# Optimization experiments

Measured on AMD Instinct MI355X. Metric: run time of the kernel, lower is better.

Reference implementation:

```python
import jax, jax.numpy as jnp
import numpy as np

NEG = -1e6  # mask value used by d2l-style masked_softmax


def masked_softmax(scores, valid_lens):
    # scores: [B, Q, K]; valid_lens: [B] int — mask key positions j >= valid_len
    K = scores.shape[-1]
    mask = jnp.arange(K, dtype=jnp.int32)[None, None, :] < valid_lens[:, None, None]
    scores = jnp.where(mask, scores, NEG)
    return jax.nn.softmax(scores, axis=-1)


def setup_inputs() -> dict:
    key = jax.random.key(0)
    kq, kk, kv, kl = jax.random.split(key, 4)
    B, Q, K, d = 16, 4096, 4096, 128
    queries = jax.random.normal(kq, (B, Q, d), dtype=jnp.float32)
    keys = jax.random.normal(kk, (B, K, d), dtype=jnp.float32)
    values = jax.random.normal(kv, (B, K, d), dtype=jnp.float32)
    valid_lens = jax.random.randint(kl, (B,), 1, K + 1, dtype=jnp.int32)
    return {"queries": queries, "keys": keys, "values": values,
            "valid_lens": valid_lens}


def reference(queries, keys, values, valid_lens):
    d = queries.shape[-1]
    # [B, Q, K] scores = Q K^T / sqrt(d)
    scores = jnp.einsum('bqd,bkd->bqk', queries, keys) / jnp.sqrt(
        jnp.asarray(d, queries.dtype))
    attn = masked_softmax(scores, valid_lens)
    # dropout is identity in eval mode
    return jnp.einsum('bqk,bkd->bqd', attn, values)
```

## Files before the change

kernel.cpp:

```cpp
#include <hip/hip_runtime.h>
#include <stdint.h>

typedef __attribute__((ext_vector_type(8))) short short8;
typedef __attribute__((ext_vector_type(4))) float float4v;

#define B_  16
#define S_  4096
#define D_  128
#define TM  64
#define TN  64
#define NT_ (S_ / TN)
#define IMG 8192

__device__ __forceinline__ unsigned short f2bf(float f) {
    union { float f; uint32_t u; } c; c.f = f;
    uint32_t u = c.u + 0x7FFFu + ((c.u >> 16) & 1u);
    return (unsigned short)(u >> 16);
}

__device__ __forceinline__ uint4 pack8(float4v x, float4v y) {
    uint4 r;
    r.x = (uint32_t)f2bf(x[0]) | ((uint32_t)f2bf(x[1]) << 16);
    r.y = (uint32_t)f2bf(x[2]) | ((uint32_t)f2bf(x[3]) << 16);
    r.z = (uint32_t)f2bf(y[0]) | ((uint32_t)f2bf(y[1]) << 16);
    r.w = (uint32_t)f2bf(y[2]) | ((uint32_t)f2bf(y[3]) << 16);
    return r;
}

__device__ __forceinline__ void gload16(const unsigned short* g, unsigned short* l) {
    __builtin_amdgcn_global_load_lds(
        (const __attribute__((address_space(1))) unsigned int*)g,
        (__attribute__((address_space(3))) unsigned int*)l, 16, 0, 0);
}

__global__ __launch_bounds__(256)
void prepass(const float* __restrict__ Kg, const float* __restrict__ Vg,
             unsigned short* __restrict__ Kb, unsigned short* __restrict__ Vb)
{
    __shared__ __align__(16) unsigned short Vimg[IMG];
    const int t = threadIdx.x;
    const int tile = blockIdx.x, b = blockIdx.y;
    const size_t img = (size_t)(b * NT_ + tile) * IMG;

    {
        const float* src = Kg + ((size_t)b * S_ + tile * TN) * D_;
        unsigned short* dst = Kb + img;
        #pragma unroll
        for (int i = 0; i < 4; ++i) {
            int bid = i * 256 + t;
            int row = bid >> 4, cbp = bid & 15;
            int cb  = cbp ^ (row & 7);
            const float* s = src + row * D_ + cb * 8;
            float4v x = *(const float4v*)s;
            float4v y = *(const float4v*)(s + 4);
            *(uint4*)(dst + (size_t)bid * 8) = pack8(x, y);
        }
    }
    {
        const float* src = Vg + ((size_t)b * S_ + tile * TN) * D_;
        #pragma unroll
        for (int i = 0; i < 8; ++i) {
            int e = (i * 256 + t) * 4;
            int k = e >> 7, c = e & 127;
            float4v v = *(const float4v*)(src + e);
            #pragma unroll
            for (int j = 0; j < 4; ++j) {
                int dr = c + j;
                int cbp = (k >> 3) ^ (dr & 7);
                Vimg[dr * TN + cbp * 8 + (k & 7)] = f2bf(v[j]);
            }
        }
        __syncthreads();
        unsigned short* dst = Vb + img;
        #pragma unroll
        for (int i = 0; i < 4; ++i) {
            int o = (i * 256 + t) * 8;
            *(uint4*)(dst + o) = *(const uint4*)(&Vimg[o]);
        }
    }
}

__global__ __launch_bounds__(256, 4)
void attn_fwd(const float* __restrict__ Qg,
              const unsigned short* __restrict__ Kb,
              const unsigned short* __restrict__ Vb,
              const int* __restrict__ VL,
              float* __restrict__ Og)
{
    __shared__ __align__(16) unsigned short Ks[TN * D_];
    __shared__ __align__(16) unsigned short Vt[D_ * TN];
    __shared__ __align__(16) unsigned short Ps[4 * 16 * 64];

    const int t    = threadIdx.x;
    const int wave = t >> 6;
    const int lane = t & 63;
    const int l16  = lane & 15;
    const int quad = lane >> 4;
    const int sw   = l16 & 7;

    const int b  = blockIdx.y;
    const int q0 = blockIdx.x * TM;
    const int nvalid = VL[b];
    const int ntiles = (nvalid + TN - 1) / TN;

    const float scale = 0.08838834764831845f;

    short8 qf[4];
    {
        const float* qp = Qg + ((size_t)b * S_ + (q0 + wave * 16 + l16)) * D_;
        #pragma unroll
        for (int ks = 0; ks < 4; ++ks) {
            float4v x = *(const float4v*)(qp + ks * 32 + quad * 8);
            float4v y = *(const float4v*)(qp + ks * 32 + quad * 8 + 4);
            #pragma unroll
            for (int j = 0; j < 4; ++j) { x[j] *= scale; y[j] *= scale; }
            union { uint4 u; short8 s; } cv; cv.u = pack8(x, y);
            qf[ks] = cv.s;
        }
    }

    float4v oacc[8];
    #pragma unroll
    for (int dt = 0; dt < 8; ++dt) oacc[dt] = (float4v){0.f, 0.f, 0.f, 0.f};
    float lsum[4] = {0.f, 0.f, 0.f, 0.f};

    unsigned short* Pw = Ps + wave * (16 * 64);

    for (int tile = 0; tile < ntiles; ++tile) {
        const int n0 = tile * TN;
        __syncthreads();

        {
            const unsigned short* kimg = Kb + (size_t)(b * NT_ + tile) * IMG;
            const unsigned short* vimg = Vb + (size_t)(b * NT_ + tile) * IMG;
            #pragma unroll
            for (int i = 0; i < 4; ++i) {
                int go = (i * 256 + t) * 8;
                int lo = (i * 256 + wave * 64) * 8;
                gload16(kimg + go, &Ks[lo]);
                gload16(vimg + go, &Vt[lo]);
            }
        }
        __syncthreads();

        float sv[4][4];
        #pragma unroll
        for (int nt = 0; nt < 4; ++nt) {
            float4v sa = (float4v){0.f, 0.f, 0.f, 0.f};
            #pragma unroll
            for (int ks = 0; ks < 4; ++ks) {
                short8 bf = *(const short8*)(&Ks[(nt * 16 + l16) * D_ + (((ks << 2) + quad) ^ sw) * 8]);
                sa = __builtin_amdgcn_mfma_f32_16x16x32_bf16(qf[ks], bf, sa, 0, 0, 0);
            }
            #pragma unroll
            for (int r = 0; r < 4; ++r) sv[nt][r] = sa[r];
        }

        const bool full = (n0 + TN) <= nvalid;
        #pragma unroll
        for (int nt = 0; nt < 4; ++nt) {
            const bool ok = full || (n0 + nt * 16 + l16) < nvalid;
            const int cb = nt * 2 + (l16 >> 3);
            #pragma unroll
            for (int r = 0; r < 4; ++r) {
                float p = ok ? __expf(sv[nt][r]) : 0.0f;
                lsum[r] += p;
                const int row = quad * 4 + r;
                Pw[row * 64 + ((cb ^ (row >> 1)) << 3) + sw] = f2bf(p);
            }
        }

        #pragma unroll
        for (int ks2 = 0; ks2 < 2; ++ks2) {
            short8 pf = *(const short8*)(&Pw[l16 * 64 + ((((ks2 << 2) + quad) ^ (l16 >> 1)) << 3)]);
            #pragma unroll
            for (int dt = 0; dt < 8; ++dt) {
                short8 vf = *(const short8*)(&Vt[(dt * 16 + l16) * TN + ((((ks2 << 2) + quad) ^ sw) << 3)]);
                oacc[dt] = __builtin_amdgcn_mfma_f32_16x16x32_bf16(pf, vf, oacc[dt], 0, 0, 0);
            }
        }
    }

    float invl[4];
    #pragma unroll
    for (int r = 0; r < 4; ++r) {
        float s = lsum[r];
        #pragma unroll
        for (int off = 1; off < 16; off <<= 1)
            s += __shfl_xor(s, off);
        invl[r] = 1.0f / s;
    }

    float* op = Og + ((size_t)b * S_ + (q0 + wave * 16 + quad * 4)) * D_;
    #pragma unroll
    for (int r = 0; r < 4; ++r) {
        #pragma unroll
        for (int dt = 0; dt < 8; ++dt)
            op[r * D_ + dt * 16 + l16] = oacc[dt][r] * invl[r];
    }
}

extern "C" void kernel_launch(void* const* d_in, const int* in_sizes, int n_in,
                              void* d_out, int out_size, void* d_ws, size_t ws_size,
                              hipStream_t stream) {
    const float* Q = (const float*)d_in[0];
    const float* K = (const float*)d_in[1];
    const float* V = (const float*)d_in[2];
    const int*   L = (const int*)d_in[3];
    float*       O = (float*)d_out;

    unsigned short* Kb = (unsigned short*)d_ws;
    unsigned short* Vb = Kb + (size_t)B_ * S_ * D_;

    dim3 grid(NT_, B_);
    prepass<<<grid, 256, 0, stream>>>(K, V, Kb, Vb);
    dim3 grid2(S_ / TM, B_);
    attn_fwd<<<grid2, 256, 0, stream>>>(Q, Kb, Vb, L, O);
}
```

Baseline: 228.8 us.

## Use 32x32 MFMA with 128-row Q tiles and shared P tile across waves

After: 307.0 us. 1.34x slower.

```diff
diff --git a/kernel.cpp b/kernel.cpp
--- a/kernel.cpp
+++ b/kernel.cpp
@@ -1,13 +1,14 @@
 #include <hip/hip_runtime.h>
 #include <stdint.h>
 
-typedef __attribute__((ext_vector_type(8))) short short8;
-typedef __attribute__((ext_vector_type(4))) float float4v;
+typedef __attribute__((ext_vector_type(8)))  short short8;
+typedef __attribute__((ext_vector_type(4)))  float float4v;
+typedef __attribute__((ext_vector_type(16))) float f32x16;
 
 #define B_  16
 #define S_  4096
 #define D_  128
-#define TM  64
+#define TM  128
 #define TN  64
 #define NT_ (S_ / TN)
 #define IMG 8192
@@ -37,7 +38,6 @@
 void prepass(const float* __restrict__ Kg, const float* __restrict__ Vg,
              unsigned short* __restrict__ Kb, unsigned short* __restrict__ Vb)
 {
-    __shared__ __align__(16) unsigned short Vimg[IMG];
     const int t = threadIdx.x;
     const int tile = blockIdx.x, b = blockIdx.y;
     const size_t img = (size_t)(b * NT_ + tile) * IMG;
@@ -51,36 +51,32 @@
             int row = bid >> 4, cbp = bid & 15;
             int cb  = cbp ^ (row & 7);
             const float* s = src + row * D_ + cb * 8;
-            float4v x = *(const float4v*)s;
-            float4v y = *(const float4v*)(s + 4);
-            *(uint4*)(dst + (size_t)bid * 8) = pack8(x, y);
+            *(uint4*)(dst + (size_t)bid * 8) = pack8(*(const float4v*)s,
+                                                     *(const float4v*)(s + 4));
         }
     }
     {
         const float* src = Vg + ((size_t)b * S_ + tile * TN) * D_;
-        #pragma unroll
-        for (int i = 0; i < 8; ++i) {
-            int e = (i * 256 + t) * 4;
-            int k = e >> 7, c = e & 127;
-            float4v v = *(const float4v*)(src + e);
-            #pragma unroll
-            for (int j = 0; j < 4; ++j) {
-                int dr = c + j;
-                int cbp = (k >> 3) ^ (dr & 7);
-                Vimg[dr * TN + cbp * 8 + (k & 7)] = f2bf(v[j]);
-            }
-        }
-        __syncthreads();
         unsigned short* dst = Vb + img;
         #pragma unroll
-        for (int i = 0; i < 4; ++i) {
-            int o = (i * 256 + t) * 8;
-            *(uint4*)(dst + o) = *(const uint4*)(&Vimg[o]);
-        }
-    }
-}
-
-__global__ __launch_bounds__(256, 4)
+        for (int it = 0; it < 4; ++it) {
+            int item = it * 256 + t;
+            int dr = item & 127, kb = item >> 7;
+            const float* p = src + (size_t)(kb * 8) * D_ + dr;
+            float v[8];
+            #pragma unroll
+            for (int i = 0; i < 8; ++i) v[i] = p[(size_t)i * D_];
+            uint4 r;
+            r.x = (uint32_t)f2bf(v[0]) | ((uint32_t)f2bf(v[1]) << 16);
+            r.y = (uint32_t)f2bf(v[2]) | ((uint32_t)f2bf(v[3]) << 16);
+            r.z = (uint32_t)f2bf(v[4]) | ((uint32_t)f2bf(v[5]) << 16);
+            r.w = (uint32_t)f2bf(v[6]) | ((uint32_t)f2bf(v[7]) << 16);
+            *(uint4*)(dst + dr * 64 + ((kb ^ (dr & 7)) << 3)) = r;
+        }
+    }
+}
+
+__global__ __launch_bounds__(256, 3)
 void attn_fwd(const float* __restrict__ Qg,
               const unsigned short* __restrict__ Kb,
               const unsigned short* __restrict__ Vb,
@@ -89,14 +85,15 @@
 {
     __shared__ __align__(16) unsigned short Ks[TN * D_];
     __shared__ __align__(16) unsigned short Vt[D_ * TN];
-    __shared__ __align__(16) unsigned short Ps[4 * 16 * 64];
+    __shared__ __align__(16) unsigned short Ps[TM * TN];
+    __shared__ __align__(16) float lbuf[TM];
 
     const int t    = threadIdx.x;
     const int wave = t >> 6;
     const int lane = t & 63;
-    const int l16  = lane & 15;
-    const int quad = lane >> 4;
-    const int sw   = l16 & 7;
+    const int l5   = lane & 31;
+    const int h    = lane >> 5;
+    const int swl  = l5 & 7;
 
     const int b  = blockIdx.y;
     const int q0 = blockIdx.x * TM;
@@ -105,13 +102,13 @@
 
     const float scale = 0.08838834764831845f;
 
-    short8 qf[4];
+    short8 qf[8];
     {
-        const float* qp = Qg + ((size_t)b * S_ + (q0 + wave * 16 + l16)) * D_;
-        #pragma unroll
-        for (int ks = 0; ks < 4; ++ks) {
-            float4v x = *(const float4v*)(qp + ks * 32 + quad * 8);
-            float4v y = *(const float4v*)(qp + ks * 32 + quad * 8 + 4);
+        const float* qp = Qg + ((size_t)b * S_ + (q0 + wave * 32 + l5)) * D_;
+        #pragma unroll
+        for (int ks = 0; ks < 8; ++ks) {
+            float4v x = *(const float4v*)(qp + ks * 16 + h * 8);
+            float4v y = *(const float4v*)(qp + ks * 16 + h * 8 + 4);
             #pragma unroll
             for (int j = 0; j < 4; ++j) { x[j] *= scale; y[j] *= scale; }
             union { uint4 u; short8 s; } cv; cv.u = pack8(x, y);
@@ -119,12 +116,15 @@
         }
     }
 
-    float4v oacc[8];
+    const int mi = wave >> 1, ni = wave & 1;
+    f32x16 oacc[2][2];
     #pragma unroll
-    for (int dt = 0; dt < 8; ++dt) oacc[dt] = (float4v){0.f, 0.f, 0.f, 0.f};
-    float lsum[4] = {0.f, 0.f, 0.f, 0.f};
-
-    unsigned short* Pw = Ps + wave * (16 * 64);
+    for (int mt = 0; mt < 2; ++mt)
+        #pragma unroll
+        for (int nt = 0; nt < 2; ++nt)
+            #pragma unroll
+            for (int r = 0; r < 16; ++r) oacc[mt][nt][r] = 0.f;
+    float lsum[2] = {0.f, 0.f};
 
     for (int tile = 0; tile < ntiles; ++tile) {
         const int n0 = tile * TN;
@@ -143,60 +143,76 @@
         }
         __syncthreads();
 
-        float sv[4][4];
-        #pragma unroll
-        for (int nt = 0; nt < 4; ++nt) {
-            float4v sa = (float4v){0.f, 0.f, 0.f, 0.f};
-            #pragma unroll
-            for (int ks = 0; ks < 4; ++ks) {
-                short8 bf = *(const short8*)(&Ks[(nt * 16 + l16) * D_ + (((ks << 2) + quad) ^ sw) * 8]);
-                sa = __builtin_amdgcn_mfma_f32_16x16x32_bf16(qf[ks], bf, sa, 0, 0, 0);
-            }
-            #pragma unroll
-            for (int r = 0; r < 4; ++r) sv[nt][r] = sa[r];
-        }
-
-        const bool full = (n0 + TN) <= nvalid;
-        #pragma unroll
-        for (int nt = 0; nt < 4; ++nt) {
-            const bool ok = full || (n0 + nt * 16 + l16) < nvalid;
-            const int cb = nt * 2 + (l16 >> 3);
-            #pragma unroll
-            for (int r = 0; r < 4; ++r) {
-                float p = ok ? __expf(sv[nt][r]) : 0.0f;
-                lsum[r] += p;
-                const int row = quad * 4 + r;
-                Pw[row * 64 + ((cb ^ (row >> 1)) << 3) + sw] = f2bf(p);
-            }
-        }
-
-        #pragma unroll
-        for (int ks2 = 0; ks2 < 2; ++ks2) {
-            short8 pf = *(const short8*)(&Pw[l16 * 64 + ((((ks2 << 2) + quad) ^ (l16 >> 1)) << 3)]);
-            #pragma unroll
-            for (int dt = 0; dt < 8; ++dt) {
-                short8 vf = *(const short8*)(&Vt[(dt * 16 + l16) * TN + ((((ks2 << 2) + quad) ^ sw) << 3)]);
-                oacc[dt] = __builtin_amdgcn_mfma_f32_16x16x32_bf16(pf, vf, oacc[dt], 0, 0, 0);
-            }
-        }
-    }
-
-    float invl[4];
+        #pragma unroll
+        for (int nt = 0; nt < 2; ++nt) {
+            f32x16 sa;
+            #pragma unroll
+            for (int r = 0; r < 16; ++r) sa[r] = 0.f;
+            #pragma unroll
+            for (int ks = 0; ks < 8; ++ks) {
+                short8 bf = *(const short8*)(&Ks[(nt * 32 + l5) * D_ + (((ks * 2 + h) ^ swl) << 3)]);
+                sa = __builtin_amdgcn_mfma_f32_32x32x16_bf16(qf[ks], bf, sa, 0, 0, 0);
+            }
+            const bool ok = (n0 + nt * 32 + l5) < nvalid;
+            const int cb  = nt * 4 + (l5 >> 3);
+            #pragma unroll
+            for (int r = 0; r < 16; ++r) {
+                float p = ok ? __expf(sa[r]) : 0.0f;
+                const int row = wave * 32 + (r & 3) + ((r >> 2) << 3) + (h << 2);
+                Ps[row * TN + ((cb ^ (row & 7)) << 3) + swl] = f2bf(p);
+            }
+        }
+        __syncthreads();
+
+        #pragma unroll
+        for (int ks = 0; ks < 4; ++ks) {
+            short8 pa[2];
+            #pragma unroll
+            for (int mt = 0; mt < 2; ++mt) {
+                const int row = mi * 64 + mt * 32 + l5;
+                pa[mt] = *(const short8*)(&Ps[row * TN + (((ks * 2 + h) ^ swl) << 3)]);
+                union { short8 s; uint32_t u[4]; } pc; pc.s = pa[mt];
+                #pragma unroll
+                for (int q2 = 0; q2 < 4; ++q2)
+                    lsum[mt] += __uint_as_float(pc.u[q2] << 16)
+                              + __uint_as_float(pc.u[q2] & 0xFFFF0000u);
+            }
+            #pragma unroll
+            for (int nt2 = 0; nt2 < 2; ++nt2) {
+                const int dcol = ni * 64 + nt2 * 32 + l5;
+                short8 vb = *(const short8*)(&Vt[dcol * TN + (((ks * 2 + h) ^ swl) << 3)]);
+                oacc[0][nt2] = __builtin_amdgcn_mfma_f32_32x32x16_bf16(pa[0], vb, oacc[0][nt2], 0, 0, 0);
+                oacc[1][nt2] = __builtin_amdgcn_mfma_f32_32x32x16_bf16(pa[1], vb, oacc[1][nt2], 0, 0, 0);
+            }
+        }
+    }
+
     #pragma unroll
-    for (int r = 0; r < 4; ++r) {
-        float s = lsum[r];
-        #pragma unroll
-        for (int off = 1; off < 16; off <<= 1)
-            s += __shfl_xor(s, off);
-        invl[r] = 1.0f / s;
-    }
-
-    float* op = Og + ((size_t)b * S_ + (q0 + wave * 16 + quad * 4)) * D_;
+    for (int mt = 0; mt < 2; ++mt) {
+        float l = lsum[mt] + __shfl_xor(lsum[mt], 32);
+        lbuf[mi * 64 + mt * 32 + l5] = l;
+    }
+    __syncthreads();
+
+    float* op = Og + ((size_t)b * S_ + q0) * D_;
     #pragma unroll
-    for (int r = 0; r < 4; ++r) {
-        #pragma unroll
-        for (int dt = 0; dt < 8; ++dt)
-            op[r * D_ + dt * 16 + l16] = oacc[dt][r] * invl[r];
+    for (int mt = 0; mt < 2; ++mt) {
+        float4v il[4];
+        #pragma unroll
+        for (int rr = 0; rr < 4; ++rr) {
+            float4v lv = *(const float4v*)(&lbuf[mi * 64 + mt * 32 + rr * 8 + h * 4]);
+            #pragma unroll
+            for (int j = 0; j < 4; ++j) il[rr][j] = 1.0f / lv[j];
+        }
+        #pragma unroll
+        for (int nt2 = 0; nt2 < 2; ++nt2) {
+            const int col = ni * 64 + nt2 * 32 + l5;
+            #pragma unroll
+            for (int r = 0; r < 16; ++r) {
+                const int row = mi * 64 + mt * 32 + (r & 3) + ((r >> 2) << 3) + (h << 2);
+                op[(size_t)row * D_ + col] = oacc[mt][nt2][r] * il[r >> 2][r & 3];
+            }
+        }
     }
 }
 
```

## Split key dimension across blocks with atomic accumulation and normalize pass

Applied to the files above, without the earlier changes.

New measurement: 264.5 us. +15.6%, slower.

```diff
diff --git a/kernel.cpp b/kernel.cpp
--- a/kernel.cpp
+++ b/kernel.cpp
@@ -11,6 +11,7 @@
 #define TN  64
 #define NT_ (S_ / TN)
 #define IMG 8192
+#define CK  16
 
 __device__ __forceinline__ unsigned short f2bf(float f) {
     union { float f; uint32_t u; } c; c.f = f;
@@ -37,7 +38,6 @@
 void prepass(const float* __restrict__ Kg, const float* __restrict__ Vg,
              unsigned short* __restrict__ Kb, unsigned short* __restrict__ Vb)
 {
-    __shared__ __align__(16) unsigned short Vimg[IMG];
     const int t = threadIdx.x;
     const int tile = blockIdx.x, b = blockIdx.y;
     const size_t img = (size_t)(b * NT_ + tile) * IMG;
@@ -51,31 +51,27 @@
             int row = bid >> 4, cbp = bid & 15;
             int cb  = cbp ^ (row & 7);
             const float* s = src + row * D_ + cb * 8;
-            float4v x = *(const float4v*)s;
-            float4v y = *(const float4v*)(s + 4);
-            *(uint4*)(dst + (size_t)bid * 8) = pack8(x, y);
+            *(uint4*)(dst + (size_t)bid * 8) = pack8(*(const float4v*)s,
+                                                     *(const float4v*)(s + 4));
         }
     }
     {
         const float* src = Vg + ((size_t)b * S_ + tile * TN) * D_;
-        #pragma unroll
-        for (int i = 0; i < 8; ++i) {
-            int e = (i * 256 + t) * 4;
-            int k = e >> 7, c = e & 127;
-            float4v v = *(const float4v*)(src + e);
-            #pragma unroll
-            for (int j = 0; j < 4; ++j) {
-                int dr = c + j;
-                int cbp = (k >> 3) ^ (dr & 7);
-                Vimg[dr * TN + cbp * 8 + (k & 7)] = f2bf(v[j]);
-            }
-        }
-        __syncthreads();
         unsigned short* dst = Vb + img;
         #pragma unroll
-        for (int i = 0; i < 4; ++i) {
-            int o = (i * 256 + t) * 8;
-            *(uint4*)(dst + o) = *(const uint4*)(&Vimg[o]);
+        for (int it = 0; it < 4; ++it) {
+            int item = it * 256 + t;
+            int dr = item & 127, kb = item >> 7;
+            const float* p = src + (size_t)(kb * 8) * D_ + dr;
+            float v[8];
+            #pragma unroll
+            for (int i = 0; i < 8; ++i) v[i] = p[(size_t)i * D_];
+            uint4 r;
+            r.x = (uint32_t)f2bf(v[0]) | ((uint32_t)f2bf(v[1]) << 16);
+            r.y = (uint32_t)f2bf(v[2]) | ((uint32_t)f2bf(v[3]) << 16);
+            r.z = (uint32_t)f2bf(v[4]) | ((uint32_t)f2bf(v[5]) << 16);
+            r.w = (uint32_t)f2bf(v[6]) | ((uint32_t)f2bf(v[7]) << 16);
+            *(uint4*)(dst + dr * 64 + ((kb ^ (dr & 7)) << 3)) = r;
         }
     }
 }
@@ -85,11 +81,21 @@
               const unsigned short* __restrict__ Kb,
               const unsigned short* __restrict__ Vb,
               const int* __restrict__ VL,
-              float* __restrict__ Og)
+              float* __restrict__ Og,
+              float* __restrict__ lbuf)
 {
     __shared__ __align__(16) unsigned short Ks[TN * D_];
     __shared__ __align__(16) unsigned short Vt[D_ * TN];
     __shared__ __align__(16) unsigned short Ps[4 * 16 * 64];
+
+    const int b  = blockIdx.y;
+    const int nvalid = VL[b];
+    const int ntiles = (nvalid + TN - 1) / TN;
+    const int ci = blockIdx.z;
+    const int t0 = ci * CK;
+    if (t0 >= ntiles) return;
+    const int t1 = (t0 + CK < ntiles) ? (t0 + CK) : ntiles;
+    const bool single = (ntiles <= CK);
 
     const int t    = threadIdx.x;
     const int wave = t >> 6;
@@ -97,11 +103,7 @@
     const int l16  = lane & 15;
     const int quad = lane >> 4;
     const int sw   = l16 & 7;
-
-    const int b  = blockIdx.y;
-    const int q0 = blockIdx.x * TM;
-    const int nvalid = VL[b];
-    const int ntiles = (nvalid + TN - 1) / TN;
+    const int q0   = blockIdx.x * TM;
 
     const float scale = 0.08838834764831845f;
 
@@ -126,7 +128,7 @@
 
     unsigned short* Pw = Ps + wave * (16 * 64);
 
-    for (int tile = 0; tile < ntiles; ++tile) {
+    for (int tile = t0; tile < t1; ++tile) {
         const int n0 = tile * TN;
         __syncthreads();
 
@@ -166,38 +168,72 @@
                 float p = ok ? __expf(sv[nt][r]) : 0.0f;
                 lsum[r] += p;
                 const int row = quad * 4 + r;
-                Pw[row * 64 + ((cb ^ (row >> 1)) << 3) + sw] = f2bf(p);
+                Ps[wave * 1024 + row * 64 + ((cb ^ (row >> 1)) << 3) + sw] = f2bf(p);
             }
         }
 
-        #pragma unroll
-        for (int ks2 = 0; ks2 < 2; ++ks2) {
-            short8 pf = *(const short8*)(&Pw[l16 * 64 + ((((ks2 << 2) + quad) ^ (l16 >> 1)) << 3)]);
-            #pragma unroll
-            for (int dt = 0; dt < 8; ++dt) {
-                short8 vf = *(const short8*)(&Vt[(dt * 16 + l16) * TN + ((((ks2 << 2) + quad) ^ sw) << 3)]);
-                oacc[dt] = __builtin_amdgcn_mfma_f32_16x16x32_bf16(pf, vf, oacc[dt], 0, 0, 0);
-            }
-        }
-    }
-
-    float invl[4];
+        short8 pf0 = *(const short8*)(&Pw[l16 * 64 + (((quad) ^ (l16 >> 1)) << 3)]);
+        short8 pf1 = *(const short8*)(&Pw[l16 * 64 + (((4 + quad) ^ (l16 >> 1)) << 3)]);
+        #pragma unroll
+        for (int dt = 0; dt < 8; ++dt) {
+            int col = dt * 16 + l16;
+            int swc = 8 * (col & 7);
+            short8 vf0 = *(const short8*)(&Vt[col * TN + ((quad * 8) ^ swc)]);
+            short8 vf1 = *(const short8*)(&Vt[col * TN + ((32 + quad * 8) ^ swc)]);
+            oacc[dt] = __builtin_amdgcn_mfma_f32_16x16x32_bf16(pf0, vf0, oacc[dt], 0, 0, 0);
+            oacc[dt] = __builtin_amdgcn_mfma_f32_16x16x32_bf16(pf1, vf1, oacc[dt], 0, 0, 0);
+        }
+    }
+
+    float lred[4];
     #pragma unroll
     for (int r = 0; r < 4; ++r) {
         float s = lsum[r];
         #pragma unroll
         for (int off = 1; off < 16; off <<= 1)
             s += __shfl_xor(s, off);
-        invl[r] = 1.0f / s;
+        lred[r] = s;
     }
 
     float* op = Og + ((size_t)b * S_ + (q0 + wave * 16 + quad * 4)) * D_;
+    if (single) {
+        #pragma unroll
+        for (int r = 0; r < 4; ++r) {
+            float invl = 1.0f / lred[r];
+            #pragma unroll
+            for (int dt = 0; dt < 8; ++dt)
+                op[r * D_ + dt * 16 + l16] = oacc[dt][r] * invl;
+        }
+    } else {
+        #pragma unroll
+        for (int r = 0; r < 4; ++r) {
+            #pragma unroll
+            for (int dt = 0; dt < 8; ++dt)
+                atomicAdd(&op[r * D_ + dt * 16 + l16], oacc[dt][r]);
+        }
+        if (l16 == 0) {
+            #pragma unroll
+            for (int r = 0; r < 4; ++r)
+                atomicAdd(&lbuf[b * S_ + q0 + wave * 16 + quad * 4 + r], lred[r]);
+        }
+    }
+}
+
+__global__ __launch_bounds__(256)
+void normalize(float* __restrict__ Og, const float* __restrict__ lbuf,
+               const int* __restrict__ VL)
+{
+    const int f = blockIdx.x * 256 + threadIdx.x;
+    const int b = f >> 17;
+    const int ntiles = (VL[b] + TN - 1) / TN;
+    if (ntiles <= CK) return;
+    const int row = (f & 131071) >> 5;
+    const float inv = 1.0f / lbuf[b * S_ + row];
+    float4v* p = (float4v*)Og;
+    float4v v = p[f];
     #pragma unroll
-    for (int r = 0; r < 4; ++r) {
-        #pragma unroll
-        for (int dt = 0; dt < 8; ++dt)
-            op[r * D_ + dt * 16 + l16] = oacc[dt][r] * invl[r];
-    }
+    for (int j = 0; j < 4; ++j) v[j] *= inv;
+    p[f] = v;
 }
 
 extern "C" void kernel_launch(void* const* d_in, const int* in_sizes, int n_in,
@@ -211,9 +247,16 @@
 
     unsigned short* Kb = (unsigned short*)d_ws;
     unsigned short* Vb = Kb + (size_t)B_ * S_ * D_;
+    float* lbuf = (float*)(Vb + (size_t)B_ * S_ * D_);
+
+    hipMemsetAsync(O, 0, (size_t)out_size * sizeof(float), stream);
+    hipMemsetAsync(lbuf, 0, (size_t)B_ * S_ * sizeof(float), stream);
 
     dim3 grid(NT_, B_);
     prepass<<<grid, 256, 0, stream>>>(K, V, Kb, Vb);
-    dim3 grid2(S_ / TM, B_);
-    attn_fwd<<<grid2, 256, 0, stream>>>(Q, Kb, Vb, L, O);
-}
+
+    dim3 grid2(S_ / TM, B_, 4);
+    attn_fwd<<<grid2, 256, 0, stream>>>(Q, Kb, Vb, L, O, lbuf);
+
+    normalize<<<(out_size / 4 + 255) / 256, 256, 0, stream>>>(O, lbuf, L);
+}
```
